# Optimization experiments

Measured on AMD Instinct MI355X. Metric: run time of the kernel, lower is better.

The kernel has to match this reference:

```python
import jax, jax.numpy as jnp
import numpy as np

K = 3
STRIDE = 1
PAD = K // 2
GN_GROUPS = 32
EPS = 1e-5


def _conv(x, w, b, stride, pad):
    y = jax.lax.conv_general_dilated(
        x, w, window_strides=(stride, stride),
        padding=[(pad, pad), (pad, pad)],
        dimension_numbers=("NCHW", "OIHW", "NCHW"))
    return y + b[None, :, None, None]


def _bilinear_gather(img, ys, xs):
    # img: [B,C,H,W]; ys/xs: [B,P,Ho,Wo] float sampling coords (zero padding outside)
    B, C, H, W = img.shape
    y0 = jnp.floor(ys)
    x0 = jnp.floor(xs)
    y1, x1 = y0 + 1.0, x0 + 1.0
    wy1 = ys - y0  # weight toward y1
    wx1 = xs - x0
    wy0 = 1.0 - wy1
    wx0 = 1.0 - wx1
    img_flat = img.reshape(B, C, H * W)

    def corner(yc, xc, wgt):
        yi = yc.astype(jnp.int32)
        xi = xc.astype(jnp.int32)
        valid = (yi >= 0) & (yi < H) & (xi >= 0) & (xi < W)
        idx = jnp.clip(yi, 0, H - 1) * W + jnp.clip(xi, 0, W - 1)  # [B,P,Ho,Wo]
        Bp, P, Ho, Wo = idx.shape
        idx_f = jnp.broadcast_to(idx.reshape(B, 1, P * Ho * Wo), (B, C, P * Ho * Wo))
        vals = jnp.take_along_axis(img_flat, idx_f, axis=2).reshape(B, C, P, Ho, Wo)
        w_eff = jnp.where(valid, wgt, 0.0)[:, None]  # [B,1,P,Ho,Wo]
        return vals * w_eff

    out = (corner(y0, x0, wy0 * wx0) + corner(y0, x1, wy0 * wx1)
           + corner(y1, x0, wy1 * wx0) + corner(y1, x1, wy1 * wx1))
    return out  # [B,C,P,Ho,Wo]


def _deform_conv_gn_relu(x, w_off, b_off, w, b, gamma, beta):
    B, C_in, H, W = x.shape
    C_out = w.shape[0]
    P = K * K
    # offset-predicting conv: [B, 2*P, Ho, Wo], channel order (dy0,dx0,dy1,dx1,...)
    off = _conv(x, w_off, b_off, STRIDE, PAD)
    Ho, Wo = off.shape[2], off.shape[3]
    off = off.reshape(B, P, 2, Ho, Wo)
    dy, dx = off[:, :, 0], off[:, :, 1]  # [B,P,Ho,Wo]
    ky, kx = jnp.meshgrid(jnp.arange(K, dtype=x.dtype), jnp.arange(K, dtype=x.dtype), indexing="ij")
    ky, kx = ky.reshape(P), kx.reshape(P)
    base_y = (jnp.arange(Ho, dtype=x.dtype) * STRIDE - PAD)
    base_x = (jnp.arange(Wo, dtype=x.dtype) * STRIDE - PAD)
    ys = base_y[None, None, :, None] + ky[None, :, None, None] + dy
    xs = base_x[None, None, None, :] + kx[None, :, None, None] + dx
    cols = _bilinear_gather(x, ys, xs)  # [B,C_in,P,Ho,Wo]
    y = jnp.einsum("bcphw,ocp->bohw", cols, w.reshape(C_out, C_in, P)) + b[None, :, None, None]
    # GroupNorm(32, C_out)
    G = GN_GROUPS
    yg = y.reshape(B, G, (C_out // G) * Ho * Wo)
    mu = yg.mean(axis=2, keepdims=True)
    var = yg.var(axis=2, keepdims=True)
    yn = ((yg - mu) * jax.lax.rsqrt(var + EPS)).reshape(B, C_out, Ho, Wo)
    yn = yn * gamma[None, :, None, None] + beta[None, :, None, None]
    return jax.nn.relu(yn)


def setup_inputs() -> dict:
    key = jax.random.key(0)
    ks = jax.random.split(key, 7)
    B, C_in, C_out, H, W = 4, 256, 256, 64, 64
    P = K * K
    fan = C_in * P
    x = jax.random.normal(ks[0], (B, C_in, H, W), dtype=jnp.float32)
    w_off = jax.random.normal(ks[1], (2 * P, C_in, K, K), dtype=jnp.float32) * 0.01
    b_off = jnp.zeros((2 * P,), dtype=jnp.float32)
    w = jax.random.normal(ks[2], (C_out, C_in, K, K), dtype=jnp.float32) / np.sqrt(fan)
    b = jax.random.normal(ks[3], (C_out,), dtype=jnp.float32) * 0.01
    gamma = jnp.ones((C_out,), dtype=jnp.float32)
    beta = jnp.zeros((C_out,), dtype=jnp.float32)
    return {"x": x, "w_off": w_off, "b_off": b_off, "w": w, "b": b, "gamma": gamma, "beta": beta}


def reference(x, w_off, b_off, w, b, gamma, beta):
    return _deform_conv_gn_relu(x, w_off, b_off, w, b, gamma, beta)
```

## Files before the change

### kernel.cpp

```cpp
#include <hip/hip_runtime.h>
#include <hip/hip_bf16.h>

using bf16 = __hip_bfloat16;
typedef __attribute__((ext_vector_type(4))) float f32x4;
typedef __attribute__((ext_vector_type(2))) float f32x2;
typedef __attribute__((ext_vector_type(8))) __bf16 bf16x8;
typedef __attribute__((ext_vector_type(4))) __bf16 bf16x4;

#define CIN 256
#define COUT 256
#define HW 4096
#define NB 4
#define NTOT 16384
#define KDIM 2304

__global__ __launch_bounds__(256) void k_transpose(const float* __restrict__ x,
                                                   float* __restrict__ xt) {
  __shared__ float t[32][33];
  int bid = blockIdx.x;
  int ct = bid & 7;
  int hwt = (bid >> 3) & 127;
  int b = bid >> 10;
  int tx = threadIdx.x & 31, ty = threadIdx.x >> 5;
  int c0 = ct * 32, hw0 = hwt * 32;
  const float* xb = x + (size_t)b * CIN * HW;
#pragma unroll
  for (int i = 0; i < 32; i += 8)
    t[ty + i][tx] = xb[(size_t)(c0 + ty + i) * HW + hw0 + tx];
  __syncthreads();
  float* xo = xt + ((size_t)b * HW + hw0) * CIN + c0;
#pragma unroll
  for (int i = 0; i < 32; i += 8)
    xo[(size_t)(ty + i) * CIN + tx] = t[tx][ty + i];
}

__global__ __launch_bounds__(256) void k_prep(const float* __restrict__ w,
                                              const float* __restrict__ wof,
                                              bf16* __restrict__ A,
                                              float* __restrict__ wt) {
  int bid = blockIdx.x;
  if (bid < 2304) {
    int i = bid * 256 + threadIdx.x;
    int o = i / KDIM, r = i % KDIM;
    int p = r >> 8, c = r & 255;
    A[i] = __float2bfloat16(w[((size_t)o * 256 + c) * 9 + p]);
  } else {
    int i = (bid - 2304) * 256 + threadIdx.x;
    if (i < 18 * CIN * 9) {
      int oc = i % 18;
      int cp = i / 18;
      int c = cp / 9, p = cp % 9;
      wt[i] = wof[((size_t)oc * CIN + c) * 9 + p];
    }
  }
}

__global__ __launch_bounds__(256) void k_convoff2(const float* __restrict__ x,
                                                  const float* __restrict__ wt,
                                                  float* __restrict__ part) {
  __shared__ float lds[8][6][68];
  int bid = blockIdx.x;
  int chunk = bid & 7;
  int rt = (bid >> 3) & 15;
  int b = bid >> 7;
  int tid = threadIdx.x;
  int wq = tid & 63, r = tid >> 6;
  int h0 = rt * 4;
  int c0 = chunk * 32;

  if (tid < 96) {
    int cl = tid / 12, rem = tid % 12;
    lds[cl][rem >> 1][(rem & 1) ? 66 : 1] = 0.f;
  }

  float acc[18];
#pragma unroll
  for (int o = 0; o < 18; ++o) acc[o] = 0.f;

  int ch = tid >> 5, l32 = tid & 31;
  const float* xb = x + (size_t)b * CIN * HW;

  for (int cs = 0; cs < 32; cs += 8) {
    __syncthreads();
    const float* xp = xb + (size_t)(c0 + cs + ch) * HW;
#pragma unroll
    for (int r6 = 0; r6 < 6; ++r6) {
      int hh = h0 - 1 + r6;
      f32x2 v = {0.f, 0.f};
      if ((unsigned)hh < 64u) v = *(const f32x2*)(xp + hh * 64 + l32 * 2);
      *(f32x2*)&lds[ch][r6][2 + l32 * 2] = v;
    }
    __syncthreads();
#pragma unroll
    for (int cl = 0; cl < 8; ++cl) {
      int c = c0 + cs + cl;
      const float* wc = wt + (size_t)c * 9 * 18;
      float xv[9];
#pragma unroll
      for (int ky = 0; ky < 3; ++ky)
#pragma unroll
        for (int kx = 0; kx < 3; ++kx)
          xv[ky * 3 + kx] = lds[cl][r + ky][1 + wq + kx];
#pragma unroll
      for (int p = 0; p < 9; ++p)
#pragma unroll
        for (int o = 0; o < 18; ++o)
          acc[o] = fmaf(xv[p], wc[p * 18 + o], acc[o]);
    }
  }

  float* pp = part + (size_t)chunk * (NB * 18 * HW) + (size_t)b * 18 * HW +
              (h0 + r) * 64 + wq;
#pragma unroll
  for (int o = 0; o < 18; ++o) pp[(size_t)o * HW] = acc[o];
}

__global__ __launch_bounds__(256) void k_offreduce(const float* __restrict__ part,
                                                   const float* __restrict__ boff,
                                                   float* __restrict__ off) {
  int i = blockIdx.x * 256 + threadIdx.x;
  int e0 = i * 4;
  int oc = (e0 >> 12) % 18;
  float bo = boff[oc];
  f32x4 s = {bo, bo, bo, bo};
#pragma unroll
  for (int c = 0; c < 8; ++c) s += *(const f32x4*)(part + (size_t)c * (NB * 18 * HW) + e0);
  *(f32x4*)(off + e0) = s;
}

__global__ __launch_bounds__(256) void k_gather(const float* __restrict__ xt,
                                                const float* __restrict__ off,
                                                bf16* __restrict__ colsT) {
  int tid = threadIdx.x;
  int wv = tid >> 6, l = tid & 63;
  int n = blockIdx.x * 4 + wv;
  int hw = n & 4095;
  int b = n >> 12;
  int h = hw >> 6, wq = hw & 63;
  const float* xtb = xt + (size_t)b * HW * CIN + l * 4;
  const float* offb = off + (size_t)b * 18 * HW + hw;
  bf16* outp = colsT + (size_t)n * KDIM + l * 4;
#pragma unroll
  for (int p = 0; p < 9; ++p) {
    float dy = offb[(size_t)(2 * p) * HW];
    float dx = offb[(size_t)(2 * p + 1) * HW];
    float ysf = (float)(h - 1 + p / 3) + dy;
    float xsf = (float)(wq - 1 + p % 3) + dx;
    float y0f = floorf(ysf), x0f = floorf(xsf);
    float wy1 = ysf - y0f, wx1 = xsf - x0f;
    float wy0 = 1.f - wy1, wx0 = 1.f - wx1;
    int y0 = (int)y0f, x0 = (int)x0f;
    int y1 = y0 + 1, x1 = x0 + 1;
    float w00 = wy0 * wx0, w01 = wy0 * wx1, w10 = wy1 * wx0, w11 = wy1 * wx1;
    bool vy0 = (unsigned)y0 < 64u, vy1 = (unsigned)y1 < 64u;
    bool vx0 = (unsigned)x0 < 64u, vx1 = (unsigned)x1 < 64u;
    w00 = (vy0 && vx0) ? w00 : 0.f;
    w01 = (vy0 && vx1) ? w01 : 0.f;
    w10 = (vy1 && vx0) ? w10 : 0.f;
    w11 = (vy1 && vx1) ? w11 : 0.f;
    int y0c = min(max(y0, 0), 63), y1c = min(max(y1, 0), 63);
    int x0c = min(max(x0, 0), 63), x1c = min(max(x1, 0), 63);
    f32x4 v00 = *(const f32x4*)(xtb + (size_t)(y0c * 64 + x0c) * CIN);
    f32x4 v01 = *(const f32x4*)(xtb + (size_t)(y0c * 64 + x1c) * CIN);
    f32x4 v10 = *(const f32x4*)(xtb + (size_t)(y1c * 64 + x0c) * CIN);
    f32x4 v11 = *(const f32x4*)(xtb + (size_t)(y1c * 64 + x1c) * CIN);
    f32x4 v;
#pragma unroll
    for (int k = 0; k < 4; ++k)
      v[k] = w00 * v00[k] + w01 * v01[k] + w10 * v10[k] + w11 * v11[k];
    bf16x4 o;
#pragma unroll
    for (int k = 0; k < 4; ++k) o[k] = (__bf16)v[k];
    *(bf16x4*)(outp + p * 256) = o;
  }
}

__global__ __launch_bounds__(256) void k_gemm(const bf16* __restrict__ A,
                                              const bf16* __restrict__ Bt,
                                              const float* __restrict__ bias,
                                              float* __restrict__ Y,
                                              float* __restrict__ gsum,
                                              float* __restrict__ gsq) {
  __shared__ bf16 As[2][64 * 64];
  __shared__ bf16 Bs[2][64 * 64];
  int bid = blockIdx.x;
  int swz = (bid & 7) * 128 + (bid >> 3);
  int mt = swz & 3, nt = swz >> 2;
  int m0 = mt * 64, n0 = nt * 64;
  int tid = threadIdx.x;
  int lane = tid & 63;
  int wave = tid >> 6;
  int wm = (wave >> 1) * 32, wn = (wave & 1) * 32;
  f32x4 acc[2][2];
#pragma unroll
  for (int i = 0; i < 2; ++i)
#pragma unroll
    for (int j = 0; j < 2; ++j) acc[i][j] = (f32x4){0.f, 0.f, 0.f, 0.f};

  int srow = tid >> 3;
  int skdst = (tid & 7) * 8;
  int sksrc = ((tid & 7) ^ ((tid >> 3) & 7)) * 8;
  auto stage = [&](int buf, int k0) {
#pragma unroll
    for (int ps = 0; ps < 2; ++ps) {
      int r = srow + ps * 32;
      __builtin_amdgcn_global_load_lds(
          (const __attribute__((address_space(1))) void*)(A + (size_t)(m0 + r) * KDIM + k0 + sksrc),
          (__attribute__((address_space(3))) void*)(&As[buf][r * 64 + skdst]), 16, 0, 0);
      __builtin_amdgcn_global_load_lds(
          (const __attribute__((address_space(1))) void*)(Bt + (size_t)(n0 + r) * KDIM + k0 + sksrc),
          (__attribute__((address_space(3))) void*)(&Bs[buf][r * 64 + skdst]), 16, 0, 0);
    }
  };

  stage(0, 0);
  int rl = lane & 15;
  int kb = (lane >> 4) * 8;
  int xorv = (rl & 7) * 8;
  constexpr int NT = KDIM / 64;
  for (int kt = 0; kt < NT; ++kt) {
    __syncthreads();
    if (kt + 1 < NT) stage((kt + 1) & 1, (kt + 1) * 64);
    const bf16* as = As[kt & 1];
    const bf16* bs = Bs[kt & 1];
#pragma unroll
    for (int kh = 0; kh < 2; ++kh) {
      int kc = (kh * 32 + kb) ^ xorv;
      bf16x8 af[2], bfr[2];
#pragma unroll
      for (int i = 0; i < 2; ++i)
        af[i] = *(const bf16x8*)(as + (wm + i * 16 + rl) * 64 + kc);
#pragma unroll
      for (int j = 0; j < 2; ++j)
        bfr[j] = *(const bf16x8*)(bs + (wn + j * 16 + rl) * 64 + kc);
#pragma unroll
      for (int i = 0; i < 2; ++i)
#pragma unroll
        for (int j = 0; j < 2; ++j)
          acc[i][j] = __builtin_amdgcn_mfma_f32_16x16x32_bf16(af[i], bfr[j], acc[i][j], 0, 0, 0);
    }
  }

  int cl = lane & 15, rg = (lane >> 4) * 4;
  int b = n0 >> 12;
#pragma unroll
  for (int i = 0; i < 2; ++i) {
    int obase = m0 + wm + i * 16;
    int ob = obase + rg;
    float s = 0.f, s2 = 0.f;
#pragma unroll
    for (int j = 0; j < 2; ++j) {
      int nn = n0 + wn + j * 16 + cl;
#pragma unroll
      for (int r = 0; r < 4; ++r) {
        float yv = acc[i][j][r] + bias[ob + r];
        Y[(size_t)(ob + r) * NTOT + nn] = yv;
        s += yv;
        s2 = fmaf(yv, yv, s2);
      }
    }
#pragma unroll
    for (int mk = 1; mk <= 16; mk <<= 1) {
      s += __shfl_xor(s, mk);
      s2 += __shfl_xor(s2, mk);
    }
    if ((lane & 31) == 0) {
      int g = (obase >> 3) + (lane >> 5);
      atomicAdd(&gsum[b * 32 + g], s);
      atomicAdd(&gsq[b * 32 + g], s2);
    }
  }
}

__global__ __launch_bounds__(256) void k_apply(const float* __restrict__ Y,
                                               const float* __restrict__ gsum,
                                               const float* __restrict__ gsq,
                                               const float* __restrict__ gamma,
                                               const float* __restrict__ beta,
                                               float* __restrict__ out) {
  int i = blockIdx.x * 256 + threadIdx.x;
  int hw4 = i & 1023;
  int o = (i >> 10) & 255;
  int b = i >> 18;
  int g = o >> 3;
  float mu = gsum[b * 32 + g] * (1.f / 32768.f);
  float var = gsq[b * 32 + g] * (1.f / 32768.f) - mu * mu;
  float rs = rsqrtf(var + 1e-5f);
  float s = rs * gamma[o];
  float t = beta[o] - mu * s;
  f32x4 v = *(const f32x4*)(Y + (size_t)o * NTOT + b * HW + hw4 * 4);
  f32x4 r;
#pragma unroll
  for (int k = 0; k < 4; ++k) r[k] = fmaxf(v[k] * s + t, 0.f);
  *(f32x4*)(out + (size_t)i * 4) = r;
}

extern "C" void kernel_launch(void* const* d_in, const int* in_sizes, int n_in,
                              void* d_out, int out_size, void* d_ws, size_t ws_size,
                              hipStream_t stream) {
  const float* x = (const float*)d_in[0];
  const float* w_off = (const float*)d_in[1];
  const float* b_off = (const float*)d_in[2];
  const float* w = (const float*)d_in[3];
  const float* bias = (const float*)d_in[4];
  const float* gamma = (const float*)d_in[5];
  const float* beta = (const float*)d_in[6];
  float* out = (float*)d_out;
  char* ws = (char*)d_ws;

  float* xt = (float*)(ws);
  float* offb = (float*)(ws + 16777216);
  bf16* Abf = (bf16*)(ws + 16777216 + 1179648);
  bf16* colsT = (bf16*)(ws + 16777216 + 2 * 1179648);
  float* Y = (float*)(ws + 16777216 + 2 * 1179648 + 75497472);
  float* gsum = (float*)(ws + 2 * 16777216 + 2 * 1179648 + 75497472);
  float* gsq = gsum + 128;

  float* wt = (float*)colsT;
  float* part = (float*)((char*)colsT + 262144);

  hipMemsetAsync(gsum, 0, 2 * 128 * sizeof(float), stream);
  k_transpose<<<4096, 256, 0, stream>>>(x, xt);
  k_prep<<<2466, 256, 0, stream>>>(w, w_off, Abf, wt);
  k_convoff2<<<512, 256, 0, stream>>>(x, wt, part);
  k_offreduce<<<288, 256, 0, stream>>>(part, b_off, offb);
  k_gather<<<4096, 256, 0, stream>>>(xt, offb, colsT);
  k_gemm<<<1024, 256, 0, stream>>>(Abf, colsT, bias, Y, gsum, gsq);
  k_apply<<<4096, 256, 0, stream>>>(Y, gsum, gsq, gamma, beta, out);
}
```

Measured before the change: 146.3 us.

## Store transposed input and GEMM output in bf16, enlarge GEMM M tile

```diff
diff --git a/kernel.cpp b/kernel.cpp
--- a/kernel.cpp
+++ b/kernel.cpp
@@ -15,23 +15,25 @@
 #define KDIM 2304
 
 __global__ __launch_bounds__(256) void k_transpose(const float* __restrict__ x,
-                                                   float* __restrict__ xt) {
-  __shared__ float t[32][33];
+                                                   bf16* __restrict__ xt) {
+  __shared__ float t[64][33];
   int bid = blockIdx.x;
-  int ct = bid & 7;
-  int hwt = (bid >> 3) & 127;
-  int b = bid >> 10;
-  int tx = threadIdx.x & 31, ty = threadIdx.x >> 5;
-  int c0 = ct * 32, hw0 = hwt * 32;
+  int ct = bid & 3;
+  int hwt = (bid >> 2) & 127;
+  int b = bid >> 9;
+  int tid = threadIdx.x;
+  int c0 = ct * 64, hw0 = hwt * 32;
   const float* xb = x + (size_t)b * CIN * HW;
-#pragma unroll
-  for (int i = 0; i < 32; i += 8)
-    t[ty + i][tx] = xb[(size_t)(c0 + ty + i) * HW + hw0 + tx];
+  int cc = tid >> 5, ww = tid & 31;
+#pragma unroll
+  for (int pass = 0; pass < 8; ++pass)
+    t[cc + pass * 8][ww] = xb[(size_t)(c0 + cc + pass * 8) * HW + hw0 + ww];
   __syncthreads();
-  float* xo = xt + ((size_t)b * HW + hw0) * CIN + c0;
-#pragma unroll
-  for (int i = 0; i < 32; i += 8)
-    xo[(size_t)(ty + i) * CIN + tx] = t[tx][ty + i];
+  int hwl = tid >> 3, ce = (tid & 7) * 8;
+  bf16x8 v;
+#pragma unroll
+  for (int e = 0; e < 8; ++e) v[e] = (__bf16)t[ce + e][hwl];
+  *(bf16x8*)(xt + ((size_t)b * HW + hw0 + hwl) * CIN + c0 + ce) = v;
 }
 
 __global__ __launch_bounds__(256) void k_prep(const float* __restrict__ w,
@@ -128,7 +130,7 @@
   *(f32x4*)(off + e0) = s;
 }
 
-__global__ __launch_bounds__(256) void k_gather(const float* __restrict__ xt,
+__global__ __launch_bounds__(256) void k_gather(const bf16* __restrict__ xt,
                                                 const float* __restrict__ off,
                                                 bf16* __restrict__ colsT) {
   int tid = threadIdx.x;
@@ -137,7 +139,7 @@
   int hw = n & 4095;
   int b = n >> 12;
   int h = hw >> 6, wq = hw & 63;
-  const float* xtb = xt + (size_t)b * HW * CIN + l * 4;
+  const bf16* xtb = xt + (size_t)b * HW * CIN + l * 4;
   const float* offb = off + (size_t)b * 18 * HW + hw;
   bf16* outp = colsT + (size_t)n * KDIM + l * 4;
 #pragma unroll
@@ -160,17 +162,17 @@
     w11 = (vy1 && vx1) ? w11 : 0.f;
     int y0c = min(max(y0, 0), 63), y1c = min(max(y1, 0), 63);
     int x0c = min(max(x0, 0), 63), x1c = min(max(x1, 0), 63);
-    f32x4 v00 = *(const f32x4*)(xtb + (size_t)(y0c * 64 + x0c) * CIN);
-    f32x4 v01 = *(const f32x4*)(xtb + (size_t)(y0c * 64 + x1c) * CIN);
-    f32x4 v10 = *(const f32x4*)(xtb + (size_t)(y1c * 64 + x0c) * CIN);
-    f32x4 v11 = *(const f32x4*)(xtb + (size_t)(y1c * 64 + x1c) * CIN);
-    f32x4 v;
-#pragma unroll
-    for (int k = 0; k < 4; ++k)
-      v[k] = w00 * v00[k] + w01 * v01[k] + w10 * v10[k] + w11 * v11[k];
+    bf16x4 c00 = *(const bf16x4*)(xtb + (size_t)(y0c * 64 + x0c) * CIN);
+    bf16x4 c01 = *(const bf16x4*)(xtb + (size_t)(y0c * 64 + x1c) * CIN);
+    bf16x4 c10 = *(const bf16x4*)(xtb + (size_t)(y1c * 64 + x0c) * CIN);
+    bf16x4 c11 = *(const bf16x4*)(xtb + (size_t)(y1c * 64 + x1c) * CIN);
     bf16x4 o;
 #pragma unroll
-    for (int k = 0; k < 4; ++k) o[k] = (__bf16)v[k];
+    for (int k = 0; k < 4; ++k) {
+      float v = w00 * (float)c00[k] + w01 * (float)c01[k] +
+                w10 * (float)c10[k] + w11 * (float)c11[k];
+      o[k] = (__bf16)v;
+    }
     *(bf16x4*)(outp + p * 256) = o;
   }
 }
@@ -178,22 +180,22 @@
 __global__ __launch_bounds__(256) void k_gemm(const bf16* __restrict__ A,
                                               const bf16* __restrict__ Bt,
                                               const float* __restrict__ bias,
-                                              float* __restrict__ Y,
+                                              bf16* __restrict__ Y,
                                               float* __restrict__ gsum,
                                               float* __restrict__ gsq) {
-  __shared__ bf16 As[2][64 * 64];
+  __shared__ bf16 As[2][128 * 64];
   __shared__ bf16 Bs[2][64 * 64];
   int bid = blockIdx.x;
-  int swz = (bid & 7) * 128 + (bid >> 3);
-  int mt = swz & 3, nt = swz >> 2;
-  int m0 = mt * 64, n0 = nt * 64;
+  int swz = (bid & 7) * 64 + (bid >> 3);
+  int mt = swz & 1, nt = swz >> 1;
+  int m0 = mt * 128, n0 = nt * 64;
   int tid = threadIdx.x;
   int lane = tid & 63;
   int wave = tid >> 6;
-  int wm = (wave >> 1) * 32, wn = (wave & 1) * 32;
-  f32x4 acc[2][2];
-#pragma unroll
-  for (int i = 0; i < 2; ++i)
+  int wr = (wave >> 1) * 64, wc = (wave & 1) * 32;
+  f32x4 acc[4][2];
+#pragma unroll
+  for (int i = 0; i < 4; ++i)
 #pragma unroll
     for (int j = 0; j < 2; ++j) acc[i][j] = (f32x4){0.f, 0.f, 0.f, 0.f};
 
@@ -202,11 +204,15 @@
   int sksrc = ((tid & 7) ^ ((tid >> 3) & 7)) * 8;
   auto stage = [&](int buf, int k0) {
 #pragma unroll
-    for (int ps = 0; ps < 2; ++ps) {
+    for (int ps = 0; ps < 4; ++ps) {
       int r = srow + ps * 32;
       __builtin_amdgcn_global_load_lds(
           (const __attribute__((address_space(1))) void*)(A + (size_t)(m0 + r) * KDIM + k0 + sksrc),
           (__attribute__((address_space(3))) void*)(&As[buf][r * 64 + skdst]), 16, 0, 0);
+    }
+#pragma unroll
+    for (int ps = 0; ps < 2; ++ps) {
+      int r = srow + ps * 32;
       __builtin_amdgcn_global_load_lds(
           (const __attribute__((address_space(1))) void*)(Bt + (size_t)(n0 + r) * KDIM + k0 + sksrc),
           (__attribute__((address_space(3))) void*)(&Bs[buf][r * 64 + skdst]), 16, 0, 0);
@@ -226,15 +232,15 @@
 #pragma unroll
     for (int kh = 0; kh < 2; ++kh) {
       int kc = (kh * 32 + kb) ^ xorv;
-      bf16x8 af[2], bfr[2];
-#pragma unroll
-      for (int i = 0; i < 2; ++i)
-        af[i] = *(const bf16x8*)(as + (wm + i * 16 + rl) * 64 + kc);
+      bf16x8 af[4], bfr[2];
+#pragma unroll
+      for (int i = 0; i < 4; ++i)
+        af[i] = *(const bf16x8*)(as + (wr + i * 16 + rl) * 64 + kc);
 #pragma unroll
       for (int j = 0; j < 2; ++j)
-        bfr[j] = *(const bf16x8*)(bs + (wn + j * 16 + rl) * 64 + kc);
-#pragma unroll
-      for (int i = 0; i < 2; ++i)
+        bfr[j] = *(const bf16x8*)(bs + (wc + j * 16 + rl) * 64 + kc);
+#pragma unroll
+      for (int i = 0; i < 4; ++i)
 #pragma unroll
         for (int j = 0; j < 2; ++j)
           acc[i][j] = __builtin_amdgcn_mfma_f32_16x16x32_bf16(af[i], bfr[j], acc[i][j], 0, 0, 0);
@@ -243,18 +249,20 @@
 
   int cl = lane & 15, rg = (lane >> 4) * 4;
   int b = n0 >> 12;
-#pragma unroll
-  for (int i = 0; i < 2; ++i) {
-    int obase = m0 + wm + i * 16;
-    int ob = obase + rg;
+  __syncthreads();
+  bf16* ytile = &As[0][0];
+#pragma unroll
+  for (int i = 0; i < 4; ++i) {
+    int obase = wr + i * 16;
+    int ob = m0 + obase + rg;
     float s = 0.f, s2 = 0.f;
 #pragma unroll
     for (int j = 0; j < 2; ++j) {
-      int nn = n0 + wn + j * 16 + cl;
+      int nl = wc + j * 16 + cl;
 #pragma unroll
       for (int r = 0; r < 4; ++r) {
         float yv = acc[i][j][r] + bias[ob + r];
-        Y[(size_t)(ob + r) * NTOT + nn] = yv;
+        ytile[(obase + rg + r) * 72 + nl] = __float2bfloat16(yv);
         s += yv;
         s2 = fmaf(yv, yv, s2);
       }
@@ -265,34 +273,46 @@
       s2 += __shfl_xor(s2, mk);
     }
     if ((lane & 31) == 0) {
-      int g = (obase >> 3) + (lane >> 5);
+      int g = ((m0 + obase) >> 3) + (lane >> 5);
       atomicAdd(&gsum[b * 32 + g], s);
       atomicAdd(&gsq[b * 32 + g], s2);
     }
   }
-}
-
-__global__ __launch_bounds__(256) void k_apply(const float* __restrict__ Y,
+  __syncthreads();
+#pragma unroll
+  for (int it = 0; it < 4; ++it) {
+    int row = wave * 32 + it * 8 + (lane >> 3);
+    int seg = (lane & 7) * 8;
+    bf16x8 v = *(const bf16x8*)&ytile[row * 72 + seg];
+    *(bf16x8*)(Y + (size_t)(m0 + row) * NTOT + n0 + seg) = v;
+  }
+}
+
+__global__ __launch_bounds__(256) void k_apply(const bf16* __restrict__ Y,
                                                const float* __restrict__ gsum,
                                                const float* __restrict__ gsq,
                                                const float* __restrict__ gamma,
                                                const float* __restrict__ beta,
                                                float* __restrict__ out) {
   int i = blockIdx.x * 256 + threadIdx.x;
-  int hw4 = i & 1023;
-  int o = (i >> 10) & 255;
-  int b = i >> 18;
+  int hw8 = i & 511;
+  int o = (i >> 9) & 255;
+  int b = i >> 17;
   int g = o >> 3;
   float mu = gsum[b * 32 + g] * (1.f / 32768.f);
   float var = gsq[b * 32 + g] * (1.f / 32768.f) - mu * mu;
   float rs = rsqrtf(var + 1e-5f);
   float s = rs * gamma[o];
   float t = beta[o] - mu * s;
-  f32x4 v = *(const f32x4*)(Y + (size_t)o * NTOT + b * HW + hw4 * 4);
-  f32x4 r;
-#pragma unroll
-  for (int k = 0; k < 4; ++k) r[k] = fmaxf(v[k] * s + t, 0.f);
-  *(f32x4*)(out + (size_t)i * 4) = r;
+  bf16x8 y = *(const bf16x8*)(Y + (size_t)o * NTOT + b * HW + hw8 * 8);
+  float* op = out + ((size_t)b * COUT + o) * HW + hw8 * 8;
+  f32x4 r0, r1;
+#pragma unroll
+  for (int k = 0; k < 4; ++k) r0[k] = fmaxf((float)y[k] * s + t, 0.f);
+#pragma unroll
+  for (int k = 0; k < 4; ++k) r1[k] = fmaxf((float)y[k + 4] * s + t, 0.f);
+  *(f32x4*)op = r0;
+  *(f32x4*)(op + 4) = r1;
 }
 
 extern "C" void kernel_launch(void* const* d_in, const int* in_sizes, int n_in,
@@ -308,23 +328,23 @@
   float* out = (float*)d_out;
   char* ws = (char*)d_ws;
 
-  float* xt = (float*)(ws);
-  float* offb = (float*)(ws + 16777216);
-  bf16* Abf = (bf16*)(ws + 16777216 + 1179648);
-  bf16* colsT = (bf16*)(ws + 16777216 + 2 * 1179648);
-  float* Y = (float*)(ws + 16777216 + 2 * 1179648 + 75497472);
-  float* gsum = (float*)(ws + 2 * 16777216 + 2 * 1179648 + 75497472);
+  bf16* xt = (bf16*)(ws);
+  float* offb = (float*)(ws + 8388608);
+  bf16* Abf = (bf16*)(ws + 8388608 + 1179648);
+  bf16* colsT = (bf16*)(ws + 8388608 + 2 * 1179648);
+  bf16* Y = (bf16*)(ws + 8388608 + 2 * 1179648 + 75497472);
+  float* gsum = (float*)(ws + 2 * 8388608 + 2 * 1179648 + 75497472);
   float* gsq = gsum + 128;
 
   float* wt = (float*)colsT;
   float* part = (float*)((char*)colsT + 262144);
 
   hipMemsetAsync(gsum, 0, 2 * 128 * sizeof(float), stream);
-  k_transpose<<<4096, 256, 0, stream>>>(x, xt);
+  k_transpose<<<2048, 256, 0, stream>>>(x, xt);
   k_prep<<<2466, 256, 0, stream>>>(w, w_off, Abf, wt);
   k_convoff2<<<512, 256, 0, stream>>>(x, wt, part);
   k_offreduce<<<288, 256, 0, stream>>>(part, b_off, offb);
   k_gather<<<4096, 256, 0, stream>>>(xt, offb, colsT);
-  k_gemm<<<1024, 256, 0, stream>>>(Abf, colsT, bias, Y, gsum, gsq);
-  k_apply<<<4096, 256, 0, stream>>>(Y, gsum, gsq, gamma, beta, out);
-}
+  k_gemm<<<512, 256, 0, stream>>>(Abf, colsT, bias, Y, gsum, gsq);
+  k_apply<<<2048, 256, 0, stream>>>(Y, gsum, gsq, gamma, beta, out);
+}
```

After: 156.0 us. 1.07x slower.
